# Kernel optimization log

Hardware: AMD Instinct MI355X
Metric: run time of the kernel (lower is better)

The kernel has to match this reference:

```python
import jax, jax.numpy as jnp
import numpy as np

H = 1024      # hidden_dim == memory_dim (required by seq-axis concat)
M = 1024      # memory_dim
FF = 4096     # ff_dim
WIN = 16      # window_size
SLOTS = 10    # persistent memory slots
B, S = 2, 4096
EPS_LN = 1e-5
EPS_NORM = 1e-12


def _layernorm(x, g, b):
    m = jnp.mean(x, axis=-1, keepdims=True)
    v = jnp.var(x, axis=-1, keepdims=True)
    return (x - m) / jnp.sqrt(v + EPS_LN) * g + b


def setup_inputs() -> dict:
    key = jax.random.key(0)
    ks = jax.random.split(key, 12)

    def lin_w(k, out_d, in_d):
        return jax.random.normal(k, (out_d, in_d), jnp.float32) / np.sqrt(in_d)

    return {
        "x": jax.random.normal(ks[0], (B, S, H), jnp.float32),
        "mem_W": lin_w(ks[1], M, M), "mem_b": jnp.zeros((M,), jnp.float32),
        "P": jax.random.normal(ks[2], (SLOTS, M), jnp.float32),
        "Wi": lin_w(ks[3], M, H), "bi": jnp.zeros((M,), jnp.float32),
        "Wl1": lin_w(ks[4], M, M), "bl1": jnp.zeros((M,), jnp.float32),
        "Wl2": lin_w(ks[5], M, M), "bl2": jnp.zeros((M,), jnp.float32),
        "Wo": lin_w(ks[6], H, M), "bo": jnp.zeros((H,), jnp.float32),
        "fgate": jnp.ones((1,), jnp.float32),
        "lrate": jnp.ones((1,), jnp.float32),
        "Wg": lin_w(ks[7], H, 2 * H), "bg": jnp.zeros((H,), jnp.float32),
        "W1": lin_w(ks[8], FF, H), "b1": jnp.zeros((FF,), jnp.float32),
        "W2": lin_w(ks[9], H, FF), "b2": jnp.zeros((H,), jnp.float32),
        "g1": jnp.ones((H,), jnp.float32), "be1": jnp.zeros((H,), jnp.float32),
        "g2": jnp.ones((H,), jnp.float32), "be2": jnp.zeros((H,), jnp.float32),
        "g3": jnp.ones((H,), jnp.float32), "be3": jnp.zeros((H,), jnp.float32),
    }


def reference(x, mem_W, mem_b, P, Wi, bi, Wl1, bl1, Wl2, bl2, Wo, bo,
              fgate, lrate, Wg, bg, W1, b1, W2, b2,
              g1, be1, g2, be2, g3, be3):
    b, s, h = x.shape
    # k = concat(x, persistent) along seq; v = k.clone()
    k_full = jnp.concatenate([x, jnp.broadcast_to(P, (b,) + P.shape)], axis=1)  # [B, S+SLOTS, H]

    # sit at positions >= S and are never inside the window, so only x is attended.
    idx = jnp.arange(s)[:, None] + jnp.arange(-WIN, 1)[None, :]
    valid = idx >= 0
    k_win = k_full[:, jnp.maximum(idx, 0)]
    scores = jnp.einsum('bsh,bswh->bsw', x, k_win) * (h ** -0.5)
    scores = jnp.where(valid[None], scores, -jnp.inf)
    attn_out = jnp.einsum('bsw,bswh->bsh', jax.nn.softmax(scores, axis=-1), k_win)
    x1 = _layernorm(x + attn_out, g1, be1)

    # --- neural long-term memory (key == value since v = k.clone())
    kv = k_full.reshape(-1, h)
    kn = kv / jnp.maximum(jnp.linalg.norm(kv, axis=-1, keepdims=True), EPS_NORM)
    kp = kn @ Wi.T + bi          # projected key; value_proj is identical
    vp = kp
    hdd = jax.nn.silu(kp @ Wl1.T + bl1)
    hdd = jax.nn.silu(hdd @ Wl2.T + bl2)
    pred = hdd @ mem_W.T + mem_b
    diff = pred - vp
    n, m = diff.shape
    grad_W = (2.0 / (n * m)) * diff.T @ hdd          # d mse / d mem_W
    W_new = (1.0 - fgate) * mem_W + lrate * grad_W   # test-time memory update
    mem_out = hdd @ W_new.T + mem_b
    mo = (mem_out @ Wo.T + bo).reshape(b, -1, h)[:, :s]  # align with x seq length

    # --- gated fusion + FFN
    gate = jax.nn.sigmoid(jnp.concatenate([x1, mo], axis=-1) @ Wg.T + bg)
    combined = gate * x1 + (1.0 - gate) * mo
    x2 = _layernorm(x1 + combined, g2, be2)
    ff = jax.nn.silu(x2 @ W1.T + b1) @ W2.T + b2
    return _layernorm(x2 + ff, g3, be3)
```

## Files before the change

### kernel.cpp

```cpp
#include <hip/hip_runtime.h>
#include <hip/hip_bf16.h>

#define WIN 16
#define SLOTS 10
#define SS 4096
#define NTOK 8192
#define NKV 8212
#define NPOS 4106

typedef unsigned short u16;
typedef unsigned int u32;
typedef __attribute__((ext_vector_type(8))) short short8;
typedef __attribute__((ext_vector_type(4))) float f32x4;

__device__ __forceinline__ u16 f2bf(float f){
  union { float f; u32 u; } a; a.f = f;
  u32 r = (a.u + 0x7fff + ((a.u >> 16) & 1)) >> 16;
  return (u16)r;
}
__device__ __forceinline__ float bf2f(u16 v){
  union { u32 u; float f; } a; a.u = ((u32)v) << 16;
  return a.f;
}

#define GLOAD(gp, lp) __builtin_amdgcn_global_load_lds( \
    (const __attribute__((address_space(1))) void*)(gp), \
    (__attribute__((address_space(3))) void*)(lp), 16, 0, 0)

#define FENCE_BARRIER() do { \
    __builtin_amdgcn_sched_barrier(0); \
    __builtin_amdgcn_s_barrier(); \
    __builtin_amdgcn_sched_barrier(0); \
  } while(0)

__global__ __launch_bounds__(256) void cvt_all(
    const float4* __restrict__ s0, const float4* __restrict__ s1,
    const float4* __restrict__ s2, const float4* __restrict__ s3,
    const float4* __restrict__ s4, const float4* __restrict__ s5,
    const float4* __restrict__ s6, const float4* __restrict__ s7,
    ushort4* __restrict__ d0, ushort4* __restrict__ d1,
    ushort4* __restrict__ d2, ushort4* __restrict__ d3,
    ushort4* __restrict__ d4, ushort4* __restrict__ d5,
    ushort4* __restrict__ d6, ushort4* __restrict__ d7)
{
  int i = blockIdx.x * 256 + threadIdx.x;
  const float4* s; ushort4* d; int base;
  if      (i <  262144){ s=s0; d=d0; base=0; }
  else if (i <  524288){ s=s1; d=d1; base=262144; }
  else if (i <  786432){ s=s2; d=d2; base=524288; }
  else if (i < 1048576){ s=s3; d=d3; base=786432; }
  else if (i < 1310720){ s=s4; d=d4; base=1048576; }
  else if (i < 1835008){ s=s5; d=d5; base=1310720; }
  else if (i < 2883584){ s=s6; d=d6; base=1835008; }
  else                 { s=s7; d=d7; base=2883584; }
  float4 v = s[i - base];
  ushort4 o; o.x=f2bf(v.x); o.y=f2bf(v.y); o.z=f2bf(v.z); o.w=f2bf(v.w);
  d[i - base] = o;
}

__global__ __launch_bounds__(256) void attn_kv(
    const float* __restrict__ x, const float* __restrict__ P,
    const float* __restrict__ g1, const float* __restrict__ be1,
    u16* __restrict__ x1b, u16* __restrict__ kn)
{
  const int blk = blockIdx.x;
  const int t = threadIdx.x, lane = t & 63, w = t >> 6;
  if (blk >= NTOK){
    const int r = blk - NTOK;
    const int b = r / NPOS;
    const int pos = r - b*NPOS;
    const float* src = (pos < SS) ? (x + (((size_t)b*SS + pos) << 10))
                                  : (P + ((size_t)(pos - SS) << 10));
    float4 v = ((const float4*)src)[t];
    float s2 = v.x*v.x + v.y*v.y + v.z*v.z + v.w*v.w;
    #pragma unroll
    for (int off=32; off; off>>=1) s2 += __shfl_xor(s2, off, 64);
    __shared__ float sh[4];
    if (lane == 0) sh[w] = s2;
    __syncthreads();
    float S = sh[0]+sh[1]+sh[2]+sh[3];
    float inv = 1.f / fmaxf(sqrtf(S), 1e-12f);
    ushort4 o; o.x=f2bf(v.x*inv); o.y=f2bf(v.y*inv); o.z=f2bf(v.z*inv); o.w=f2bf(v.w*inv);
    ((ushort4*)kn)[((size_t)r << 8) + t] = o;
    return;
  }
  const int n = blk;
  const int b = n >> 12, s = n & 4095;
  const float* xb = x + ((size_t)b << 22);
  const float4 q = ((const float4*)(xb + ((size_t)s << 10)))[t];
  const int j0 = (s >= WIN) ? 0 : (WIN - s);
  float kvv[17][4];
  float part[17];
  #pragma unroll
  for (int j=0;j<17;j++){
    float4 kk = make_float4(0.f,0.f,0.f,0.f);
    if (j >= j0) kk = ((const float4*)(xb + ((size_t)(s - WIN + j) << 10)))[t];
    kvv[j][0]=kk.x; kvv[j][1]=kk.y; kvv[j][2]=kk.z; kvv[j][3]=kk.w;
    part[j] = q.x*kk.x + q.y*kk.y + q.z*kk.z + q.w*kk.w;
  }
  __shared__ float red[17][4];
  #pragma unroll
  for (int j=0;j<17;j++){
    float v = part[j];
    #pragma unroll
    for (int off=32; off; off>>=1) v += __shfl_xor(v, off, 64);
    if (lane == 0) red[j][w] = v;
  }
  __syncthreads();
  __shared__ float wsh[17];
  if (t == 0){
    float sc[17];
    float mx = -3.0e38f;
    #pragma unroll
    for (int j=0;j<17;j++){
      float v = (red[j][0]+red[j][1]+red[j][2]+red[j][3]) * 0.03125f;
      sc[j] = v;
      if (j >= j0) mx = fmaxf(mx, v);
    }
    float ssum = 0.f;
    #pragma unroll
    for (int j=0;j<17;j++){
      float e = (j >= j0) ? expf(sc[j]-mx) : 0.f;
      wsh[j] = e; ssum += e;
    }
    float inv = 1.f/ssum;
    #pragma unroll
    for (int j=0;j<17;j++) wsh[j] *= inv;
  }
  __syncthreads();
  float y0=q.x, y1=q.y, y2=q.z, y3=q.w;
  #pragma unroll
  for (int j=0;j<17;j++){
    float wj = wsh[j];
    y0 += wj*kvv[j][0]; y1 += wj*kvv[j][1]; y2 += wj*kvv[j][2]; y3 += wj*kvv[j][3];
  }
  float s1 = y0+y1+y2+y3;
  float s2 = y0*y0+y1*y1+y2*y2+y3*y3;
  #pragma unroll
  for (int off=32; off; off>>=1){ s1 += __shfl_xor(s1, off, 64); s2 += __shfl_xor(s2, off, 64); }
  __shared__ float rsh[8];
  if (lane == 0){ rsh[w] = s1; rsh[4+w] = s2; }
  __syncthreads();
  float S1 = rsh[0]+rsh[1]+rsh[2]+rsh[3];
  float S2 = rsh[4]+rsh[5]+rsh[6]+rsh[7];
  float mean = S1 * (1.f/1024.f);
  float var  = S2 * (1.f/1024.f) - mean*mean;
  float rstd = 1.f/sqrtf(var + 1e-5f);
  float4 gv = ((const float4*)g1)[t];
  float4 bv = ((const float4*)be1)[t];
  ushort4 ob;
  ob.x = f2bf((y0-mean)*rstd*gv.x + bv.x);
  ob.y = f2bf((y1-mean)*rstd*gv.y + bv.y);
  ob.z = f2bf((y2-mean)*rstd*gv.z + bv.z);
  ob.w = f2bf((y3-mean)*rstd*gv.w + bv.w);
  ((ushort4*)x1b)[((size_t)n << 8) + t] = ob;
}

template<int EPI, int SPLITA>
__global__ __launch_bounds__(256) void gemm_nt(
    const u16* __restrict__ A, const u16* __restrict__ A2,
    const u16* __restrict__ Bmat, const float* __restrict__ bias,
    const u16* __restrict__ auxb,
    float* __restrict__ Cf, u16* __restrict__ Cb,
    int N, int O, int ldA, int ldB, int klen)
{
  __shared__ __align__(16) u16 lA[4][128*32];
  __shared__ __align__(16) u16 lB[4][128*32];
  const int t = threadIdx.x;
  const int lane = t & 63;
  const int bm0 = blockIdx.x * 128;
  const int bn0 = blockIdx.y * 128;
  const int wid = t >> 6;
  const int wr = wid >> 1, wc = wid & 1;
  const int nkh = klen >> 5;

  f32x4 acc[4][4];
  #pragma unroll
  for (int i=0;i<4;i++)
    #pragma unroll
    for (int j=0;j<4;j++)
      acc[i][j] = (f32x4){0.f,0.f,0.f,0.f};

  const int srow = t >> 2;
  const int sch  = t & 3;
  const int csw  = ((sch ^ ((srow >> 1) & 3)) << 3);

  int gr0 = bm0 + srow;      gr0 = gr0 < N ? gr0 : N-1;
  int gr1 = bm0 + srow + 64; gr1 = gr1 < N ? gr1 : N-1;
  int gb0 = bn0 + srow;      gb0 = gb0 < O ? gb0 : O-1;
  int gb1 = bn0 + srow + 64; gb1 = gb1 < O ? gb1 : O-1;
  const u16* bA0 = A + (size_t)gr0*(size_t)ldA + csw;
  const u16* bA1 = A + (size_t)gr1*(size_t)ldA + csw;
  const u16* bA20 = SPLITA ? (A2 + ((size_t)gr0 << 10) + csw) : nullptr;
  const u16* bA21 = SPLITA ? (A2 + ((size_t)gr1 << 10) + csw) : nullptr;
  const u16* bB0 = Bmat + (size_t)gb0*(size_t)ldB + csw;
  const u16* bB1 = Bmat + (size_t)gb1*(size_t)ldB + csw;
  const int dLo = t << 3;
  const int dHi = (t << 3) + 2048;

  auto stage = [&](int j){
    const int kb = j << 5;
    const int s = j & 3;
    const u16* a0 = SPLITA ? ((kb < 1024) ? bA0 + kb : bA20 + (kb - 1024)) : bA0 + kb;
    const u16* a1 = SPLITA ? ((kb < 1024) ? bA1 + kb : bA21 + (kb - 1024)) : bA1 + kb;
    GLOAD(a0, &lA[s][dLo]);
    GLOAD(a1, &lA[s][dHi]);
    GLOAD(bB0 + kb, &lB[s][dLo]);
    GLOAD(bB1 + kb, &lB[s][dHi]);
  };

  stage(0);
  if (nkh > 1) stage(1);
  if (nkh > 2) stage(2);

  const int l15 = lane & 15;
  const int cq  = lane >> 4;
  const int soff = ((cq ^ ((l15 >> 1) & 3)) << 3);

  for (int j = 0; j < nkh; ++j){
    const int s = j & 3;
    const int cnt = 4*((j+1 < nkh) + (j+2 < nkh));
    if (cnt == 8)      { asm volatile("s_waitcnt vmcnt(8)" ::: "memory"); }
    else if (cnt == 4) { asm volatile("s_waitcnt vmcnt(4)" ::: "memory"); }
    else               { asm volatile("s_waitcnt vmcnt(0)" ::: "memory"); }
    FENCE_BARRIER();
    short8 af[4], bfv[4];
    #pragma unroll
    for (int mi=0;mi<4;mi++)
      af[mi] = *(const short8*)(&lA[s][((wr*64 + mi*16 + l15) * 32) + soff]);
    #pragma unroll
    for (int ni=0;ni<4;ni++)
      bfv[ni] = *(const short8*)(&lB[s][((wc*64 + ni*16 + l15) * 32) + soff]);
    if (j + 3 < nkh) stage(j + 3);
    __builtin_amdgcn_sched_barrier(0);
    __builtin_amdgcn_s_setprio(1);
    #pragma unroll
    for (int mi=0;mi<4;mi++)
      #pragma unroll
      for (int ni=0;ni<4;ni++)
        acc[mi][ni] = __builtin_amdgcn_mfma_f32_16x16x32_bf16(af[mi], bfv[ni], acc[mi][ni], 0, 0, 0);
    __builtin_amdgcn_s_setprio(0);
    __builtin_amdgcn_sched_barrier(0);
  }

  const int rbase = (lane >> 4) * 4;
  const int cidx = lane & 15;
  #pragma unroll
  for (int mi=0;mi<4;mi++){
    #pragma unroll
    for (int r=0;r<4;r++){
      const int n = bm0 + wr*64 + mi*16 + rbase + r;
      if (n >= N) continue;
      #pragma unroll
      for (int ni=0;ni<4;ni++){
        const int o = bn0 + wc*64 + ni*16 + cidx;
        float v = acc[mi][ni][r] + bias[o];
        if (EPI == 6){
          int b = n / NPOS;
          int pos = n - b*NPOS;
          if (pos < SS){
            Cb[(((size_t)(b*SS + pos)) << 10) + o] = f2bf(v);
          }
        } else {
          size_t idx = (size_t)n*(size_t)O + o;
          if (EPI == 0){ Cf[idx] = v; }
          else if (EPI == 1){ float sv = v/(1.f+__expf(-v)); Cb[idx] = f2bf(sv); }
          else if (EPI == 2){ Cb[idx] = f2bf(v); }
          else if (EPI == 4){ Cb[idx] = f2bf(v - bf2f(auxb[idx])); }
          else if (EPI == 5){ Cb[idx] = f2bf(1.f/(1.f+__expf(-v))); }
        }
      }
    }
  }
}

template<int EPI>
__global__ __launch_bounds__(512, 2) void gemm_256(
    const u16* __restrict__ A, const u16* __restrict__ Bmat,
    const float* __restrict__ bias,
    float* __restrict__ Cf, float* __restrict__ Cf2, u16* __restrict__ Cb,
    int N, int O, int ldA, int ldB, int klen)
{
  __shared__ __align__(16) u16 lA[4][256*32];
  __shared__ __align__(16) u16 lB[4][256*32];
  const int t = threadIdx.x;
  const int lane = t & 63;
  const int wid = t >> 6;
  const int wr = wid >> 2, wc = wid & 3;
  const int bm0 = blockIdx.x * 256;
  const int bn0 = blockIdx.y * 256;
  const size_t koff = (size_t)blockIdx.z * (size_t)klen;
  const int nkh = klen >> 5;

  f32x4 acc[8][4];
  #pragma unroll
  for (int i=0;i<8;i++)
    #pragma unroll
    for (int j=0;j<4;j++)
      acc[i][j] = (f32x4){0.f,0.f,0.f,0.f};

  const int srow = t >> 2;
  const int sch  = t & 3;
  const int csw  = ((sch ^ ((srow >> 1) & 3)) << 3);
  int gr0 = bm0 + srow;       gr0 = gr0 < N ? gr0 : N-1;
  int gr1 = bm0 + srow + 128; gr1 = gr1 < N ? gr1 : N-1;
  int gb0 = bn0 + srow;       gb0 = gb0 < O ? gb0 : O-1;
  int gb1 = bn0 + srow + 128; gb1 = gb1 < O ? gb1 : O-1;
  const u16* baseA0 = A    + (size_t)gr0*(size_t)ldA + koff + csw;
  const u16* baseA1 = A    + (size_t)gr1*(size_t)ldA + koff + csw;
  const u16* baseB0 = Bmat + (size_t)gb0*(size_t)ldB + koff + csw;
  const u16* baseB1 = Bmat + (size_t)gb1*(size_t)ldB + koff + csw;
  const int ldsLo = srow*32 + (sch << 3);
  const int ldsHi = (srow + 128)*32 + (sch << 3);

  auto stageA = [&](int j){
    const int kb = j << 5;
    const int s = j & 3;
    GLOAD(baseA0 + kb, &lA[s][ldsLo]);
    GLOAD(baseA1 + kb, &lA[s][ldsHi]);
  };
  auto stageB = [&](int j){
    const int kb = j << 5;
    const int s = j & 3;
    GLOAD(baseB0 + kb, &lB[s][ldsLo]);
    GLOAD(baseB1 + kb, &lB[s][ldsHi]);
  };

  stageA(0); stageB(0);
  if (nkh > 1){ stageA(1); stageB(1); }
  if (nkh > 2){ stageA(2); stageB(2); }

  const int l15 = lane & 15;
  const int cq  = lane >> 4;
  const int chS = ((cq ^ ((l15 >> 1) & 3)) << 3);

  for (int j = 0; j < nkh; ++j){
    const int s = j & 3;
    const int rem = nkh - 1 - j;
    if (rem >= 2)      { asm volatile("s_waitcnt vmcnt(8)" ::: "memory"); }
    else if (rem == 1) { asm volatile("s_waitcnt vmcnt(4)" ::: "memory"); }
    else               { asm volatile("s_waitcnt vmcnt(0)" ::: "memory"); }
    FENCE_BARRIER();
    short8 af[4], bfv[4];
    #pragma unroll
    for (int ni=0;ni<4;ni++)
      bfv[ni] = *(const short8*)(&lB[s][((wc*64 + ni*16 + l15) * 32) + chS]);
    #pragma unroll
    for (int mi=0;mi<4;mi++)
      af[mi] = *(const short8*)(&lA[s][((wr*128 + mi*16 + l15) * 32) + chS]);
    if (j + 3 < nkh) stageA(j + 3);
    __builtin_amdgcn_sched_barrier(0);
    __builtin_amdgcn_s_setprio(1);
    #pragma unroll
    for (int mi=0;mi<4;mi++)
      #pragma unroll
      for (int ni=0;ni<4;ni++)
        acc[mi][ni] = __builtin_amdgcn_mfma_f32_16x16x32_bf16(af[mi], bfv[ni], acc[mi][ni], 0, 0, 0);
    __builtin_amdgcn_s_setprio(0);
    __builtin_amdgcn_sched_barrier(0);
    FENCE_BARRIER();
    #pragma unroll
    for (int mi=0;mi<4;mi++)
      af[mi] = *(const short8*)(&lA[s][((wr*128 + (mi+4)*16 + l15) * 32) + chS]);
    if (j + 3 < nkh) stageB(j + 3);
    __builtin_amdgcn_sched_barrier(0);
    __builtin_amdgcn_s_setprio(1);
    #pragma unroll
    for (int mi=0;mi<4;mi++)
      #pragma unroll
      for (int ni=0;ni<4;ni++)
        acc[mi+4][ni] = __builtin_amdgcn_mfma_f32_16x16x32_bf16(af[mi], bfv[ni], acc[mi+4][ni], 0, 0, 0);
    __builtin_amdgcn_s_setprio(0);
    __builtin_amdgcn_sched_barrier(0);
  }

  float* dstf = (EPI == 7) ? (blockIdx.z ? Cf2 : Cf) : Cf;
  const int rbase = (lane >> 4) * 4;
  const int cidx = lane & 15;
  #pragma unroll
  for (int mi=0;mi<8;mi++){
    #pragma unroll
    for (int r=0;r<4;r++){
      const int n = bm0 + wr*128 + mi*16 + rbase + r;
      if (n >= N) continue;
      #pragma unroll
      for (int ni=0;ni<4;ni++){
        const int o = bn0 + wc*64 + ni*16 + cidx;
        size_t idx = (size_t)n*(size_t)O + o;
        if (EPI == 7){ dstf[idx] = acc[mi][ni][r]; }
        else {
          float v = acc[mi][ni][r] + bias[o];
          if (EPI == 0){ Cf[idx] = v; }
          else if (EPI == 1){ float sv = v/(1.f+__expf(-v)); Cb[idx] = f2bf(sv); }
          else if (EPI == 2){ Cb[idx] = f2bf(v); }
        }
      }
    }
  }
}

#define NSPLIT 6
__global__ __launch_bounds__(256) void gemm_tn(
    const u16* __restrict__ A, const u16* __restrict__ B,
    float* __restrict__ part0, float* __restrict__ part1)
{
  __shared__ __align__(16) u16 lA[128*64];
  __shared__ __align__(16) u16 lB[128*64];
  const int t = threadIdx.x, lane = t & 63;
  const int i0 = blockIdx.x * 128, j0 = blockIdx.y * 128, z = blockIdx.z;
  const int wid = t >> 6, wr = wid >> 1, wc = wid & 1;
  const int TILES = (NKV + 63) >> 6;
  const int PER = (TILES + NSPLIT - 1) / NSPLIT;
  const int kt0 = z * PER;
  const int ktend = (kt0 + PER < TILES) ? (kt0 + PER) : TILES;

  f32x4 acc[4][4];
  #pragma unroll
  for (int i=0;i<4;i++)
    #pragma unroll
    for (int j=0;j<4;j++)
      acc[i][j] = (f32x4){0.f,0.f,0.f,0.f};

  const int p = t & 31;
  const int g = t >> 5;

  auto loadr = [&](int kt, short8 R[8]){
    const int n0 = kt << 6;
    const int na = n0 + 2*p, nb = na + 1;
    short8 z8 = (short8){0,0,0,0,0,0,0,0};
    R[0]=z8;R[1]=z8;R[2]=z8;R[3]=z8;R[4]=z8;R[5]=z8;R[6]=z8;R[7]=z8;
    if (na < NKV){
      const u16* ra = A + (size_t)na*1024 + i0 + g*16;
      R[0] = *(const short8*)ra; R[1] = *(const short8*)(ra+8);
      const u16* rb = B + (size_t)na*1024 + j0 + g*16;
      R[4] = *(const short8*)rb; R[5] = *(const short8*)(rb+8);
    }
    if (nb < NKV){
      const u16* ra = A + (size_t)nb*1024 + i0 + g*16;
      R[2] = *(const short8*)ra; R[3] = *(const short8*)(ra+8);
      const u16* rb = B + (size_t)nb*1024 + j0 + g*16;
      R[6] = *(const short8*)rb; R[7] = *(const short8*)(rb+8);
    }
  };

  short8 cr[8], nr[8];
  loadr(kt0, cr);

  const int pc = p >> 2, pl = p & 3;

  for (int kt = kt0; kt < ktend; ++kt){
    if (kt + 1 < ktend) loadr(kt + 1, nr);
    asm volatile("" ::: "memory");
    FENCE_BARRIER();
    u32* wA = (u32*)lA; u32* wB = (u32*)lB;
    #pragma unroll
    for (int e=0;e<8;e++){
      const int s = (pc ^ e) * 4 + pl;
      wA[(g*16 + e)*32 + s]     = ((u32)(u16)cr[0][e]) | (((u32)(u16)cr[2][e]) << 16);
      wB[(g*16 + e)*32 + s]     = ((u32)(u16)cr[4][e]) | (((u32)(u16)cr[6][e]) << 16);
    }
    #pragma unroll
    for (int e=0;e<8;e++){
      const int s = (pc ^ e) * 4 + pl;
      wA[(g*16 + 8 + e)*32 + s] = ((u32)(u16)cr[1][e]) | (((u32)(u16)cr[3][e]) << 16);
      wB[(g*16 + 8 + e)*32 + s] = ((u32)(u16)cr[5][e]) | (((u32)(u16)cr[7][e]) << 16);
    }
    asm volatile("s_waitcnt lgkmcnt(0)" ::: "memory");
    FENCE_BARRIER();
    const int l15 = lane & 15;
    const int rx = l15 & 7;
    const int cq = lane >> 4;
    #pragma unroll
    for (int kk=0;kk<2;kk++){
      const int soff = (((kk*4 + cq) ^ rx) << 3);
      short8 af[4], bfv[4];
      #pragma unroll
      for (int mi=0;mi<4;mi++)
        af[mi] = *(const short8*)(lA + ((wr*64 + mi*16 + l15) << 6) + soff);
      #pragma unroll
      for (int ni=0;ni<4;ni++)
        bfv[ni] = *(const short8*)(lB + ((wc*64 + ni*16 + l15) << 6) + soff);
      #pragma unroll
      for (int mi=0;mi<4;mi++)
        #pragma unroll
        for (int ni=0;ni<4;ni++)
          acc[mi][ni] = __builtin_amdgcn_mfma_f32_16x16x32_bf16(af[mi], bfv[ni], acc[mi][ni], 0, 0, 0);
    }
    #pragma unroll
    for (int e=0;e<8;e++) cr[e] = nr[e];
  }

  float* dst = (z < 4) ? (part0 + ((size_t)z << 20)) : (part1 + ((size_t)(z-4) << 20));
  const int rbase = (lane >> 4) * 4;
  const int cidx = lane & 15;
  #pragma unroll
  for (int mi=0;mi<4;mi++)
    #pragma unroll
    for (int r=0;r<4;r++){
      const int i = i0 + wr*64 + mi*16 + rbase + r;
      #pragma unroll
      for (int ni=0;ni<4;ni++){
        const int j = j0 + wc*64 + ni*16 + cidx;
        dst[((size_t)i << 10) + j] = acc[mi][ni][r];
      }
    }
}

__global__ __launch_bounds__(256) void wnew_k(const float* __restrict__ part0,
                                              const float* __restrict__ part1,
                                              const float* __restrict__ memW,
                                              const float* __restrict__ fg,
                                              const float* __restrict__ lr,
                                              u16* __restrict__ out)
{
  int i = blockIdx.x*256 + threadIdx.x;
  float s = part0[i] + part0[i + (1<<20)] + part0[i + (2<<20)] + part0[i + (3<<20)]
          + part1[i] + part1[i + (1<<20)];
  const float scale = 2.f / ((float)NKV * 1024.f);
  float v = (1.f - fg[0])*memW[i] + lr[0]*scale*s;
  out[i] = f2bf(v);
}

__global__ __launch_bounds__(256) void ln_gate(
    const u16* __restrict__ x1b, const u16* __restrict__ gateb,
    const u16* __restrict__ mob, const float* __restrict__ g2,
    const float* __restrict__ be2, u16* __restrict__ x2b)
{
  const int n = blockIdx.x;
  const int t = threadIdx.x, lane = t & 63, w = t >> 6;
  const size_t rb = (size_t)n << 8;
  ushort4 xa = ((const ushort4*)x1b)[rb+t];
  ushort4 ga = ((const ushort4*)gateb)[rb+t];
  ushort4 ma = ((const ushort4*)mob)[rb+t];
  float a0=bf2f(xa.x),a1=bf2f(xa.y),a2=bf2f(xa.z),a3=bf2f(xa.w);
  float g0=bf2f(ga.x),g1v=bf2f(ga.y),g2v=bf2f(ga.z),g3v=bf2f(ga.w);
  float m0=bf2f(ma.x),m1=bf2f(ma.y),m2=bf2f(ma.z),m3=bf2f(ma.w);
  float y0 = a0 + g0*a0 + (1.f-g0)*m0;
  float y1 = a1 + g1v*a1 + (1.f-g1v)*m1;
  float y2 = a2 + g2v*a2 + (1.f-g2v)*m2;
  float y3 = a3 + g3v*a3 + (1.f-g3v)*m3;
  float s1 = y0+y1+y2+y3;
  float s2 = y0*y0+y1*y1+y2*y2+y3*y3;
  #pragma unroll
  for (int off=32; off; off>>=1){ s1 += __shfl_xor(s1, off, 64); s2 += __shfl_xor(s2, off, 64); }
  __shared__ float rsh[8];
  if (lane == 0){ rsh[w] = s1; rsh[4+w] = s2; }
  __syncthreads();
  float S1 = rsh[0]+rsh[1]+rsh[2]+rsh[3];
  float S2 = rsh[4]+rsh[5]+rsh[6]+rsh[7];
  float mean = S1 * (1.f/1024.f);
  float var  = S2 * (1.f/1024.f) - mean*mean;
  float rstd = 1.f/sqrtf(var + 1e-5f);
  float4 gv = ((const float4*)g2)[t];
  float4 bv = ((const float4*)be2)[t];
  ushort4 ob;
  ob.x = f2bf((y0-mean)*rstd*gv.x + bv.x);
  ob.y = f2bf((y1-mean)*rstd*gv.y + bv.y);
  ob.z = f2bf((y2-mean)*rstd*gv.z + bv.z);
  ob.w = f2bf((y3-mean)*rstd*gv.w + bv.w);
  ((ushort4*)x2b)[rb + t] = ob;
}

__global__ __launch_bounds__(256) void ln_final(
    const u16* __restrict__ x2b, const float* __restrict__ g3,
    const float* __restrict__ be3, float* __restrict__ out)
{
  const int n = blockIdx.x;
  const int t = threadIdx.x, lane = t & 63, w = t >> 6;
  const size_t rb = (size_t)n << 8;
  ushort4 xa = ((const ushort4*)x2b)[rb+t];
  float4 f = ((const float4*)out)[rb+t];
  float y0 = bf2f(xa.x)+f.x, y1 = bf2f(xa.y)+f.y, y2 = bf2f(xa.z)+f.z, y3 = bf2f(xa.w)+f.w;
  float s1 = y0+y1+y2+y3;
  float s2 = y0*y0+y1*y1+y2*y2+y3*y3;
  #pragma unroll
  for (int off=32; off; off>>=1){ s1 += __shfl_xor(s1, off, 64); s2 += __shfl_xor(s2, off, 64); }
  __shared__ float rsh[8];
  if (lane == 0){ rsh[w] = s1; rsh[4+w] = s2; }
  __syncthreads();
  float S1 = rsh[0]+rsh[1]+rsh[2]+rsh[3];
  float S2 = rsh[4]+rsh[5]+rsh[6]+rsh[7];
  float mean = S1 * (1.f/1024.f);
  float var  = S2 * (1.f/1024.f) - mean*mean;
  float rstd = 1.f/sqrtf(var + 1e-5f);
  float4 gv = ((const float4*)g3)[t];
  float4 bv = ((const float4*)be3)[t];
  float4 o;
  o.x = (y0-mean)*rstd*gv.x + bv.x;
  o.y = (y1-mean)*rstd*gv.y + bv.y;
  o.z = (y2-mean)*rstd*gv.z + bv.z;
  o.w = (y3-mean)*rstd*gv.w + bv.w;
  ((float4*)out)[rb + t] = o;
}

__global__ __launch_bounds__(256) void ln_final2(
    const u16* __restrict__ x2b, const float* __restrict__ p0,
    const float* __restrict__ p1, const float* __restrict__ b2,
    const float* __restrict__ g3, const float* __restrict__ be3,
    float* __restrict__ out)
{
  const int n = blockIdx.x;
  const int t = threadIdx.x, lane = t & 63, w = t >> 6;
  const size_t rb = (size_t)n << 8;
  ushort4 xa = ((const ushort4*)x2b)[rb+t];
  float4 f0 = ((const float4*)p0)[rb+t];
  float4 f1 = ((const float4*)p1)[rb+t];
  float4 bb = ((const float4*)b2)[t];
  float y0 = bf2f(xa.x)+f0.x+f1.x+bb.x, y1 = bf2f(xa.y)+f0.y+f1.y+bb.y;
  float y2 = bf2f(xa.z)+f0.z+f1.z+bb.z, y3 = bf2f(xa.w)+f0.w+f1.w+bb.w;
  float s1 = y0+y1+y2+y3;
  float s2 = y0*y0+y1*y1+y2*y2+y3*y3;
  #pragma unroll
  for (int off=32; off; off>>=1){ s1 += __shfl_xor(s1, off, 64); s2 += __shfl_xor(s2, off, 64); }
  __shared__ float rsh[8];
  if (lane == 0){ rsh[w] = s1; rsh[4+w] = s2; }
  __syncthreads();
  float S1 = rsh[0]+rsh[1]+rsh[2]+rsh[3];
  float S2 = rsh[4]+rsh[5]+rsh[6]+rsh[7];
  float mean = S1 * (1.f/1024.f);
  float var  = S2 * (1.f/1024.f) - mean*mean;
  float rstd = 1.f/sqrtf(var + 1e-5f);
  float4 gv = ((const float4*)g3)[t];
  float4 bv = ((const float4*)be3)[t];
  float4 o;
  o.x = (y0-mean)*rstd*gv.x + bv.x;
  o.y = (y1-mean)*rstd*gv.y + bv.y;
  o.z = (y2-mean)*rstd*gv.z + bv.z;
  o.w = (y3-mean)*rstd*gv.w + bv.w;
  ((float4*)out)[rb + t] = o;
}

extern "C" void kernel_launch(void* const* d_in, const int* in_sizes, int n_in,
                              void* d_out, int out_size, void* d_ws, size_t ws_size,
                              hipStream_t stream)
{
  const float* x    = (const float*)d_in[0];
  const float* memW = (const float*)d_in[1];
  const float* memb = (const float*)d_in[2];
  const float* P    = (const float*)d_in[3];
  const float* Wi   = (const float*)d_in[4];
  const float* bi   = (const float*)d_in[5];
  const float* Wl1  = (const float*)d_in[6];
  const float* bl1  = (const float*)d_in[7];
  const float* Wl2  = (const float*)d_in[8];
  const float* bl2  = (const float*)d_in[9];
  const float* Wo   = (const float*)d_in[10];
  const float* bo   = (const float*)d_in[11];
  const float* fg   = (const float*)d_in[12];
  const float* lr   = (const float*)d_in[13];
  const float* Wg   = (const float*)d_in[14];
  const float* bg   = (const float*)d_in[15];
  const float* W1   = (const float*)d_in[16];
  const float* b1   = (const float*)d_in[17];
  const float* W2   = (const float*)d_in[18];
  const float* b2   = (const float*)d_in[19];
  const float* g1   = (const float*)d_in[20];
  const float* be1  = (const float*)d_in[21];
  const float* g2   = (const float*)d_in[22];
  const float* be2  = (const float*)d_in[23];
  const float* g3   = (const float*)d_in[24];
  const float* be3  = (const float*)d_in[25];
  float* out = (float*)d_out;

  const size_t SZ_TOK = (size_t)NTOK*1024*2;
  const size_t SZ_KV  = (size_t)NKV*1024*2;
  char* base = (char*)d_ws;
  size_t off = 0;
  auto alloc = [&](size_t bytes) -> char* {
    char* p = base + off;
    off += (bytes + 255) & ~(size_t)255;
    return p;
  };
  u16* x1b   = (u16*)alloc(SZ_TOK);
  u16* knb   = (u16*)alloc(SZ_KV);
  u16* h1b   = (u16*)alloc(SZ_KV);
  u16* hddb  = (u16*)alloc(SZ_KV);
  u16* kpb   = (u16*)alloc(SZ_KV);
  u16* wnewb = (u16*)alloc((size_t)1024*1024*2);
  u16* WiB   = (u16*)alloc((size_t)1024*1024*2);
  u16* Wl1B  = (u16*)alloc((size_t)1024*1024*2);
  u16* Wl2B  = (u16*)alloc((size_t)1024*1024*2);
  u16* memWB = (u16*)alloc((size_t)1024*1024*2);
  u16* WoB   = (u16*)alloc((size_t)1024*1024*2);
  u16* WgB   = (u16*)alloc((size_t)1024*2048*2);
  u16* W1B   = (u16*)alloc((size_t)4096*1024*2);
  u16* W2B   = (u16*)alloc((size_t)1024*4096*2);
  const size_t off_base = off;
  if (ws_size < off_base) return;

  float* ffp0 = (float*)alloc((size_t)NTOK*1024*4);
  float* ffp1 = (float*)alloc((size_t)NTOK*1024*4);
  const bool use_split_ff2 = (ws_size >= off);

  u16*   diffb   = knb;
  float* part0   = (float*)kpb;
  float* part1   = (float*)WiB;
  u16*   memoutb = knb;
  u16*   mob     = h1b;
  u16*   gateb   = hddb;
  u16*   x2b     = kpb;
  u16*   ff1b    = x1b;

  cvt_all<<<15360, 256, 0, stream>>>(
      (const float4*)Wi, (const float4*)Wl1, (const float4*)Wl2, (const float4*)memW,
      (const float4*)Wo, (const float4*)Wg, (const float4*)W1, (const float4*)W2,
      (ushort4*)WiB, (ushort4*)Wl1B, (ushort4*)Wl2B, (ushort4*)memWB,
      (ushort4*)WoB, (ushort4*)WgB, (ushort4*)W1B, (ushort4*)W2B);

  attn_kv<<<NTOK + NKV, 256, 0, stream>>>(x, P, g1, be1, x1b, knb);

  dim3 gkv(65, 8, 1);
  gemm_nt<2,0><<<gkv, 256, 0, stream>>>(knb, nullptr, WiB, bi, nullptr, nullptr, kpb, NKV, 1024, 1024, 1024, 1024);
  gemm_nt<1,0><<<gkv, 256, 0, stream>>>(kpb, nullptr, Wl1B, bl1, nullptr, nullptr, h1b, NKV, 1024, 1024, 1024, 1024);
  gemm_nt<1,0><<<gkv, 256, 0, stream>>>(h1b, nullptr, Wl2B, bl2, nullptr, nullptr, hddb, NKV, 1024, 1024, 1024, 1024);
  gemm_nt<4,0><<<gkv, 256, 0, stream>>>(hddb, nullptr, memWB, memb, kpb, nullptr, diffb, NKV, 1024, 1024, 1024, 1024);
  gemm_tn<<<dim3(8, 8, NSPLIT), 256, 0, stream>>>(diffb, hddb, part0, part1);
  wnew_k<<<4096, 256, 0, stream>>>(part0, part1, memW, fg, lr, wnewb);
  gemm_nt<2,0><<<gkv, 256, 0, stream>>>(hddb, nullptr, wnewb, memb, nullptr, nullptr, memoutb, NKV, 1024, 1024, 1024, 1024);
  gemm_nt<6,0><<<gkv, 256, 0, stream>>>(memoutb, nullptr, WoB, bo, nullptr, nullptr, mob, NKV, 1024, 1024, 1024, 1024);
  gemm_nt<5,1><<<dim3(64, 8, 1), 256, 0, stream>>>(x1b, mob, WgB, bg, nullptr, nullptr, gateb, NTOK, 1024, 1024, 2048, 2048);
  ln_gate<<<NTOK, 256, 0, stream>>>(x1b, gateb, mob, g2, be2, x2b);
  gemm_256<1><<<dim3(32, 16, 1), 512, 0, stream>>>(x2b, W1B, b1, nullptr, nullptr, ff1b, NTOK, 4096, 1024, 1024, 1024);
  if (use_split_ff2){
    gemm_256<7><<<dim3(32, 4, 2), 512, 0, stream>>>(ff1b, W2B, nullptr, ffp0, ffp1, nullptr, NTOK, 1024, 4096, 4096, 2048);
    ln_final2<<<NTOK, 256, 0, stream>>>(x2b, ffp0, ffp1, b2, g3, be3, out);
  } else {
    gemm_nt<0,0><<<dim3(64, 8, 1), 256, 0, stream>>>(ff1b, nullptr, W2B, b2, nullptr, out, nullptr, NTOK, 1024, 4096, 4096, 4096);
    ln_final<<<NTOK, 256, 0, stream>>>(x2b, g3, be3, out);
  }
}
```

Baseline: 630.0 us.

## Map one token per wavefront in attention/normalize kernel with online softmax

Restructures attn_kv so that each 64-lane wavefront handles a whole token row instead of a 256-thread block per token. All reductions become wave shuffles with no shared memory or barriers. The 17-tap window softmax now uses a streaming online-softmax accumulation, which removes the serial single-thread softmax and the large per-thread kvv register array. The trade-off is fewer threads per row and a data-dependent loop, which may lower memory-level parallelism per wave, and the non-coalesced per-lane float4 stride of 4 could hurt load efficiency.

```diff
diff --git a/kernel.cpp b/kernel.cpp
--- a/kernel.cpp
+++ b/kernel.cpp
@@ -7,6 +7,8 @@
 #define NTOK 8192
 #define NKV 8212
 #define NPOS 4106
+#define NATTB 2048
+#define NKVB 2053
 
 typedef unsigned short u16;
 typedef unsigned int u32;
@@ -21,6 +23,11 @@
 __device__ __forceinline__ float bf2f(u16 v){
   union { u32 u; float f; } a; a.u = ((u32)v) << 16;
   return a.f;
+}
+__device__ __forceinline__ float wred(float v){
+  #pragma unroll
+  for (int off=32; off; off>>=1) v += __shfl_xor(v, off, 64);
+  return v;
 }
 
 #define GLOAD(gp, lp) __builtin_amdgcn_global_load_lds( \
@@ -64,96 +71,96 @@
     u16* __restrict__ x1b, u16* __restrict__ kn)
 {
   const int blk = blockIdx.x;
-  const int t = threadIdx.x, lane = t & 63, w = t >> 6;
-  if (blk >= NTOK){
-    const int r = blk - NTOK;
+  const int t = threadIdx.x, lane = t & 63, wid = t >> 6;
+  if (blk >= NATTB){
+    const int r = (blk - NATTB)*4 + wid;
+    if (r >= NKV) return;
     const int b = r / NPOS;
     const int pos = r - b*NPOS;
-    const float* src = (pos < SS) ? (x + (((size_t)b*SS + pos) << 10))
-                                  : (P + ((size_t)(pos - SS) << 10));
-    float4 v = ((const float4*)src)[t];
-    float s2 = v.x*v.x + v.y*v.y + v.z*v.z + v.w*v.w;
-    #pragma unroll
-    for (int off=32; off; off>>=1) s2 += __shfl_xor(s2, off, 64);
-    __shared__ float sh[4];
-    if (lane == 0) sh[w] = s2;
-    __syncthreads();
-    float S = sh[0]+sh[1]+sh[2]+sh[3];
-    float inv = 1.f / fmaxf(sqrtf(S), 1e-12f);
-    ushort4 o; o.x=f2bf(v.x*inv); o.y=f2bf(v.y*inv); o.z=f2bf(v.z*inv); o.w=f2bf(v.w*inv);
-    ((ushort4*)kn)[((size_t)r << 8) + t] = o;
+    const float4* src = (const float4*)((pos < SS) ? (x + (((size_t)b*SS + pos) << 10))
+                                                   : (P + ((size_t)(pos - SS) << 10)));
+    float4 v[4];
+    float ss = 0.f;
+    #pragma unroll
+    for (int e=0;e<4;e++){
+      v[e] = src[(lane<<2)+e];
+      ss += v[e].x*v[e].x + v[e].y*v[e].y + v[e].z*v[e].z + v[e].w*v[e].w;
+    }
+    ss = wred(ss);
+    float inv = 1.f / fmaxf(sqrtf(ss), 1e-12f);
+    ushort4* dst = (ushort4*)kn + ((size_t)r << 8);
+    #pragma unroll
+    for (int e=0;e<4;e++){
+      ushort4 o; o.x=f2bf(v[e].x*inv); o.y=f2bf(v[e].y*inv); o.z=f2bf(v[e].z*inv); o.w=f2bf(v[e].w*inv);
+      dst[(lane<<2)+e] = o;
+    }
     return;
   }
-  const int n = blk;
+  const int n = blk*4 + wid;
   const int b = n >> 12, s = n & 4095;
   const float* xb = x + ((size_t)b << 22);
-  const float4 q = ((const float4*)(xb + ((size_t)s << 10)))[t];
+  const float4* qp = (const float4*)(xb + ((size_t)s << 10));
+  float4 q[4];
+  #pragma unroll
+  for (int e=0;e<4;e++) q[e] = qp[(lane<<2)+e];
+
   const int j0 = (s >= WIN) ? 0 : (WIN - s);
-  float kvv[17][4];
-  float part[17];
-  #pragma unroll
-  for (int j=0;j<17;j++){
-    float4 kk = make_float4(0.f,0.f,0.f,0.f);
-    if (j >= j0) kk = ((const float4*)(xb + ((size_t)(s - WIN + j) << 10)))[t];
-    kvv[j][0]=kk.x; kvv[j][1]=kk.y; kvv[j][2]=kk.z; kvv[j][3]=kk.w;
-    part[j] = q.x*kk.x + q.y*kk.y + q.z*kk.z + q.w*kk.w;
-  }
-  __shared__ float red[17][4];
-  #pragma unroll
-  for (int j=0;j<17;j++){
-    float v = part[j];
-    #pragma unroll
-    for (int off=32; off; off>>=1) v += __shfl_xor(v, off, 64);
-    if (lane == 0) red[j][w] = v;
-  }
-  __syncthreads();
-  __shared__ float wsh[17];
-  if (t == 0){
-    float sc[17];
-    float mx = -3.0e38f;
-    #pragma unroll
-    for (int j=0;j<17;j++){
-      float v = (red[j][0]+red[j][1]+red[j][2]+red[j][3]) * 0.03125f;
-      sc[j] = v;
-      if (j >= j0) mx = fmaxf(mx, v);
-    }
-    float ssum = 0.f;
-    #pragma unroll
-    for (int j=0;j<17;j++){
-      float e = (j >= j0) ? expf(sc[j]-mx) : 0.f;
-      wsh[j] = e; ssum += e;
-    }
-    float inv = 1.f/ssum;
-    #pragma unroll
-    for (int j=0;j<17;j++) wsh[j] *= inv;
-  }
-  __syncthreads();
-  float y0=q.x, y1=q.y, y2=q.z, y3=q.w;
-  #pragma unroll
-  for (int j=0;j<17;j++){
-    float wj = wsh[j];
-    y0 += wj*kvv[j][0]; y1 += wj*kvv[j][1]; y2 += wj*kvv[j][2]; y3 += wj*kvv[j][3];
-  }
-  float s1 = y0+y1+y2+y3;
-  float s2 = y0*y0+y1*y1+y2*y2+y3*y3;
-  #pragma unroll
-  for (int off=32; off; off>>=1){ s1 += __shfl_xor(s1, off, 64); s2 += __shfl_xor(s2, off, 64); }
-  __shared__ float rsh[8];
-  if (lane == 0){ rsh[w] = s1; rsh[4+w] = s2; }
-  __syncthreads();
-  float S1 = rsh[0]+rsh[1]+rsh[2]+rsh[3];
-  float S2 = rsh[4]+rsh[5]+rsh[6]+rsh[7];
-  float mean = S1 * (1.f/1024.f);
-  float var  = S2 * (1.f/1024.f) - mean*mean;
+  float m = -3.0e38f, l = 0.f;
+  float4 o[4];
+  #pragma unroll
+  for (int e=0;e<4;e++) o[e] = make_float4(0.f,0.f,0.f,0.f);
+
+  for (int j = j0; j < 17; ++j){
+    const float4* kp_ = (const float4*)(xb + ((size_t)(s - WIN + j) << 10));
+    float4 kk[4];
+    float dp = 0.f;
+    #pragma unroll
+    for (int e=0;e<4;e++){
+      kk[e] = kp_[(lane<<2)+e];
+      dp += q[e].x*kk[e].x + q[e].y*kk[e].y + q[e].z*kk[e].z + q[e].w*kk[e].w;
+    }
+    dp = wred(dp) * 0.03125f;
+    float mn = fmaxf(m, dp);
+    float sc = __expf(m - mn);
+    float e_ = __expf(dp - mn);
+    l = l*sc + e_;
+    #pragma unroll
+    for (int e=0;e<4;e++){
+      o[e].x = o[e].x*sc + e_*kk[e].x;
+      o[e].y = o[e].y*sc + e_*kk[e].y;
+      o[e].z = o[e].z*sc + e_*kk[e].z;
+      o[e].w = o[e].w*sc + e_*kk[e].w;
+    }
+    m = mn;
+  }
+  const float il = 1.f / l;
+  float s1 = 0.f, s2 = 0.f;
+  float4 y[4];
+  #pragma unroll
+  for (int e=0;e<4;e++){
+    y[e].x = q[e].x + o[e].x*il;
+    y[e].y = q[e].y + o[e].y*il;
+    y[e].z = q[e].z + o[e].z*il;
+    y[e].w = q[e].w + o[e].w*il;
+    s1 += y[e].x + y[e].y + y[e].z + y[e].w;
+    s2 += y[e].x*y[e].x + y[e].y*y[e].y + y[e].z*y[e].z + y[e].w*y[e].w;
+  }
+  s1 = wred(s1); s2 = wred(s2);
+  float mean = s1 * (1.f/1024.f);
+  float var  = s2 * (1.f/1024.f) - mean*mean;
   float rstd = 1.f/sqrtf(var + 1e-5f);
-  float4 gv = ((const float4*)g1)[t];
-  float4 bv = ((const float4*)be1)[t];
-  ushort4 ob;
-  ob.x = f2bf((y0-mean)*rstd*gv.x + bv.x);
-  ob.y = f2bf((y1-mean)*rstd*gv.y + bv.y);
-  ob.z = f2bf((y2-mean)*rstd*gv.z + bv.z);
-  ob.w = f2bf((y3-mean)*rstd*gv.w + bv.w);
-  ((ushort4*)x1b)[((size_t)n << 8) + t] = ob;
+  ushort4* dst = (ushort4*)x1b + ((size_t)n << 8);
+  #pragma unroll
+  for (int e=0;e<4;e++){
+    float4 gv = ((const float4*)g1)[(lane<<2)+e];
+    float4 bv = ((const float4*)be1)[(lane<<2)+e];
+    ushort4 ob;
+    ob.x = f2bf((y[e].x-mean)*rstd*gv.x + bv.x);
+    ob.y = f2bf((y[e].y-mean)*rstd*gv.y + bv.y);
+    ob.z = f2bf((y[e].z-mean)*rstd*gv.z + bv.z);
+    ob.w = f2bf((y[e].w-mean)*rstd*gv.w + bv.w);
+    dst[(lane<<2)+e] = ob;
+  }
 }
 
 template<int EPI, int SPLITA>
@@ -707,7 +714,7 @@
       (ushort4*)WiB, (ushort4*)Wl1B, (ushort4*)Wl2B, (ushort4*)memWB,
       (ushort4*)WoB, (ushort4*)WgB, (ushort4*)W1B, (ushort4*)W2B);
 
-  attn_kv<<<NTOK + NKV, 256, 0, stream>>>(x, P, g1, be1, x1b, knb);
+  attn_kv<<<NATTB + NKVB, 256, 0, stream>>>(x, P, g1, be1, x1b, knb);
 
   dim3 gkv(65, 8, 1);
   gemm_nt<2,0><<<gkv, 256, 0, stream>>>(knb, nullptr, WiB, bi, nullptr, nullptr, kpb, NKV, 1024, 1024, 1024, 1024);
```

Result: faster. 607.9 us (-3.5%).
